# Performance work log

Measured on AMD Instinct MI355X. Metric: run time of the kernel, lower is better.

Reference implementation:

```python
import jax, jax.numpy as jnp
import numpy as np

M, N, K = 4096, 8192, 4096


def setup_inputs() -> dict:
    key = jax.random.key(0)
    k1, k2, k3, k4 = jax.random.split(key, 4)
    a = jax.random.randint(k1, (M, K), 0, 127, dtype=jnp.int32)  # int8 activations
    b = jax.random.randint(k2, (N, K), 0, 127, dtype=jnp.int32)  # int8 weights (row-major [N,K])
    alpha_row = jax.random.uniform(k3, (M, 1), dtype=jnp.float16)  # per-row dequant scale
    alpha_col = jax.random.uniform(k4, (1, N), dtype=jnp.float16)  # per-col dequant scale
    return {"a": a, "b": b, "alpha_row": alpha_row, "alpha_col": alpha_col}


def reference(a, b, alpha_row, alpha_col):
    # x = a @ b.T in fp32 (int8 values upcast), then rescale by outer product of scales
    x = jnp.matmul(a.astype(jnp.float32), b.astype(jnp.float32).T)  # [M, N]
    scale = alpha_row.astype(jnp.float32) * alpha_col.astype(jnp.float32)  # [M, N] via broadcast
    out = x * scale
    return out.astype(jnp.float16)
```

## Files before the change

### kernel.cpp

```cpp
#include <hip/hip_runtime.h>
#include <cstdint>
#include <cstddef>

#define M_DIM 4096
#define N_DIM 8192
#define K_DIM 4096

typedef __attribute__((ext_vector_type(4))) int int4v;
typedef __attribute__((ext_vector_type(16))) int int16v;

__global__ void __launch_bounds__(256) pack_frag(const int* __restrict__ a,
                                                 const int* __restrict__ b,
                                                 unsigned char* __restrict__ pa,
                                                 unsigned char* __restrict__ pb) {
    size_t t = (size_t)blockIdx.x * 256 + threadIdx.x;
    const size_t NA = (size_t)(M_DIM / 32) * (K_DIM / 32) * 64;
    const int* __restrict__ src;
    unsigned char* __restrict__ dst;
    if (t < NA) {
        src = a; dst = pa;
    } else {
        src = b; dst = pb; t -= NA;
    }
    const int l = (int)(t & 63);
    const int s = (int)((t >> 6) & (K_DIM / 32 - 1));
    const int p = (int)(t >> 13);
    const int* g = src + ((size_t)(32 * p + (l & 31))) * K_DIM + s * 32 + (l >> 5) * 16;
    const int4v* g4 = (const int4v*)g;
    int4v o;
#pragma unroll
    for (int q = 0; q < 4; ++q) {
        int4v v = g4[q];
        o[q] = (v[0] & 0xff) | ((v[1] & 0xff) << 8) | ((v[2] & 0xff) << 16) | (v[3] << 24);
    }
    ((int4v*)dst)[t] = o;
}

__device__ inline void async_copy16(const unsigned char* g, unsigned char* l) {
    __builtin_amdgcn_global_load_lds(
        (const __attribute__((address_space(1))) void*)g,
        (__attribute__((address_space(3))) void*)l,
        16, 0, 0);
}

__global__ void __launch_bounds__(512, 2) gemm_i8(const unsigned char* __restrict__ Ap,
                                                  const unsigned char* __restrict__ Bp,
                                                  const _Float16* __restrict__ arow,
                                                  const _Float16* __restrict__ acol,
                                                  _Float16* __restrict__ Cout) {
    __shared__ __align__(16) unsigned char As[4 * 16384];
    __shared__ __align__(16) unsigned char Bs[4 * 16384];

    const int tid  = threadIdx.x;
    const int lane = tid & 63;
    const int wave = tid >> 6;
    const int bn   = blockIdx.x;
    const int bm   = blockIdx.y;

    const int pm0 = (wave & 3) * 2;
    const int pn0 = (wave >> 2) * 4;

    const unsigned char* ag = Ap + (size_t)(bm * 8 + wave) * 131072 + lane * 16;
    const unsigned char* bg = Bp + (size_t)(bn * 8 + wave) * 131072 + lane * 16;
    const int slo = wave * 2048;

    const int a_off = pm0 * 2048 + lane * 16;
    const int b_off = pn0 * 2048 + lane * 16;

    int16v acc[2][4];
#pragma unroll
    for (int i = 0; i < 2; ++i)
#pragma unroll
        for (int j = 0; j < 4; ++j) acc[i][j] = (int16v)0;

    const int NT = K_DIM / 64;

#pragma unroll
    for (int u = 0; u < 2; ++u) {
        async_copy16(ag + u * 1024,        As + slo + u * 1024);
        async_copy16(bg + u * 1024,        Bs + slo + u * 1024);
        async_copy16(ag + 2048 + u * 1024, As + 16384 + slo + u * 1024);
        async_copy16(bg + 2048 + u * 1024, Bs + 16384 + slo + u * 1024);
    }
    __syncthreads();

    for (int T = 0; T < NT; T += 2) {
        if (T + 2 < NT) {
#pragma unroll
            for (int w = 2; w < 4; ++w) {
                const size_t gko = (size_t)(T + w) * 2048;
                const int buf = ((T + w) & 3) * 16384;
#pragma unroll
                for (int u = 0; u < 2; ++u) {
                    async_copy16(ag + gko + u * 1024, As + buf + slo + u * 1024);
                    async_copy16(bg + gko + u * 1024, Bs + buf + slo + u * 1024);
                }
            }
        }

#pragma unroll
        for (int v = 0; v < 2; ++v) {
            const int cur = ((T + v) & 3) * 16384;
            const unsigned char* Ac = As + cur;
            const unsigned char* Bc = Bs + cur;

            int4v af[2][2], bf[2][4];
#pragma unroll
            for (int u = 0; u < 2; ++u) {
#pragma unroll
                for (int i = 0; i < 2; ++i)
                    af[u][i] = *(const int4v*)(Ac + a_off + i * 2048 + u * 1024);
#pragma unroll
                for (int j = 0; j < 4; ++j)
                    bf[u][j] = *(const int4v*)(Bc + b_off + j * 2048 + u * 1024);
            }

#pragma unroll
            for (int u = 0; u < 2; ++u)
#pragma unroll
                for (int i = 0; i < 2; ++i)
#pragma unroll
                    for (int j = 0; j < 4; ++j)
                        acc[i][j] = __builtin_amdgcn_mfma_i32_32x32x32_i8(
                            af[u][i], bf[u][j], acc[i][j], 0, 0, 0);
        }

        __syncthreads();
    }

    const int gcol0 = bn * 256 + pn0 * 32 + (lane & 31);
    float ac4[4];
#pragma unroll
    for (int j = 0; j < 4; ++j) ac4[j] = (float)acol[gcol0 + j * 32];

    const size_t rbase = (size_t)bm * 256 + pm0 * 32 + 4 * (lane >> 5);
#pragma unroll
    for (int i = 0; i < 2; ++i) {
#pragma unroll
        for (int r = 0; r < 16; ++r) {
            const size_t row = rbase + i * 32 + (r & 3) + 8 * (r >> 2);
            const float ar = (float)arow[row];
            _Float16* outp = Cout + row * (size_t)N_DIM + gcol0;
#pragma unroll
            for (int j = 0; j < 4; ++j) {
                float v = (float)acc[i][j][r] * ar * ac4[j];
                outp[j * 32] = (_Float16)v;
            }
        }
    }
}

extern "C" void kernel_launch(void* const* d_in, const int* in_sizes, int n_in,
                              void* d_out, int out_size, void* d_ws, size_t ws_size,
                              hipStream_t stream) {
    const int* a = (const int*)d_in[0];
    const int* b = (const int*)d_in[1];
    const _Float16* ar = (const _Float16*)d_in[2];
    const _Float16* ac = (const _Float16*)d_in[3];
    _Float16* out = (_Float16*)d_out;

    unsigned char* pa = (unsigned char*)d_ws;
    unsigned char* pb = pa + (size_t)M_DIM * K_DIM;

    const size_t total_frag = (size_t)(M_DIM / 32 + N_DIM / 32) * (K_DIM / 32) * 64;
    pack_frag<<<(int)(total_frag / 256), 256, 0, stream>>>(a, b, pa, pb);

    dim3 grid(N_DIM / 256, M_DIM / 256);
    gemm_i8<<<grid, 512, 0, stream>>>(pa, pb, ar, ac, out);
}
```

Measured before the change: 381.7 us.

## Use 4 waves with 128x128 warp tiles and inline-asm MFMA into AGPRs

Halves the block to 256 threads (4 waves), giving each wave a 4x4 grid of 32x32 MFMA tiles instead of 2x4, so each wave does twice the work. Each thread now issues twice as many async copies. All LDS fragments for both k-steps are loaded up front, and MFMAs are issued through inline asm that keeps accumulators in AGPRs. The aim is more MFMA work per LDS read and fewer waves. The cost is much higher register pressure, lower occupancy, and manual hazard nops before the epilogue.

```diff
diff --git a/kernel.cpp b/kernel.cpp
--- a/kernel.cpp
+++ b/kernel.cpp
@@ -43,7 +43,11 @@
         16, 0, 0);
 }
 
-__global__ void __launch_bounds__(512, 2) gemm_i8(const unsigned char* __restrict__ Ap,
+__device__ inline void mfma32(int16v& acc, int4v av, int4v bv) {
+    asm("v_mfma_i32_32x32x32_i8 %0, %1, %2, %0" : "+a"(acc) : "v"(av), "v"(bv));
+}
+
+__global__ void __launch_bounds__(256, 1) gemm_i8(const unsigned char* __restrict__ Ap,
                                                   const unsigned char* __restrict__ Bp,
                                                   const _Float16* __restrict__ arow,
                                                   const _Float16* __restrict__ acol,
@@ -57,31 +61,42 @@
     const int bn   = blockIdx.x;
     const int bm   = blockIdx.y;
 
-    const int pm0 = (wave & 3) * 2;
-    const int pn0 = (wave >> 2) * 4;
+    const int pm0 = (wave & 1) * 4;
+    const int pn0 = (wave >> 1) * 4;
 
-    const unsigned char* ag = Ap + (size_t)(bm * 8 + wave) * 131072 + lane * 16;
-    const unsigned char* bg = Bp + (size_t)(bn * 8 + wave) * 131072 + lane * 16;
-    const int slo = wave * 2048;
+    const unsigned char* ag[2];
+    const unsigned char* bg[2];
+    int slo[2];
+#pragma unroll
+    for (int r = 0; r < 2; ++r) {
+        const int p = 2 * wave + r;
+        ag[r]  = Ap + (size_t)(bm * 8 + p) * 131072 + lane * 16;
+        bg[r]  = Bp + (size_t)(bn * 8 + p) * 131072 + lane * 16;
+        slo[r] = p * 2048;
+    }
 
     const int a_off = pm0 * 2048 + lane * 16;
     const int b_off = pn0 * 2048 + lane * 16;
 
-    int16v acc[2][4];
+    int16v acc[4][4];
 #pragma unroll
-    for (int i = 0; i < 2; ++i)
+    for (int i = 0; i < 4; ++i)
 #pragma unroll
         for (int j = 0; j < 4; ++j) acc[i][j] = (int16v)0;
 
     const int NT = K_DIM / 64;
 
 #pragma unroll
-    for (int u = 0; u < 2; ++u) {
-        async_copy16(ag + u * 1024,        As + slo + u * 1024);
-        async_copy16(bg + u * 1024,        Bs + slo + u * 1024);
-        async_copy16(ag + 2048 + u * 1024, As + 16384 + slo + u * 1024);
-        async_copy16(bg + 2048 + u * 1024, Bs + 16384 + slo + u * 1024);
-    }
+    for (int t = 0; t < 2; ++t)
+#pragma unroll
+        for (int r = 0; r < 2; ++r)
+#pragma unroll
+            for (int u = 0; u < 2; ++u) {
+                async_copy16(ag[r] + t * 2048 + u * 1024,
+                             As + t * 16384 + slo[r] + u * 1024);
+                async_copy16(bg[r] + t * 2048 + u * 1024,
+                             Bs + t * 16384 + slo[r] + u * 1024);
+            }
     __syncthreads();
 
     for (int T = 0; T < NT; T += 2) {
@@ -91,42 +106,53 @@
                 const size_t gko = (size_t)(T + w) * 2048;
                 const int buf = ((T + w) & 3) * 16384;
 #pragma unroll
-                for (int u = 0; u < 2; ++u) {
-                    async_copy16(ag + gko + u * 1024, As + buf + slo + u * 1024);
-                    async_copy16(bg + gko + u * 1024, Bs + buf + slo + u * 1024);
-                }
+                for (int r = 0; r < 2; ++r)
+#pragma unroll
+                    for (int u = 0; u < 2; ++u) {
+                        async_copy16(ag[r] + gko + u * 1024, As + buf + slo[r] + u * 1024);
+                        async_copy16(bg[r] + gko + u * 1024, Bs + buf + slo[r] + u * 1024);
+                    }
             }
         }
 
+        const int c0 = (T & 3) * 16384;
+        const int c1 = ((T + 1) & 3) * 16384;
+
+        int4v a0[8], b0[8], a1[8], b1[8];
 #pragma unroll
-        for (int v = 0; v < 2; ++v) {
-            const int cur = ((T + v) & 3) * 16384;
-            const unsigned char* Ac = As + cur;
-            const unsigned char* Bc = Bs + cur;
-
-            int4v af[2][2], bf[2][4];
+        for (int i = 0; i < 4; ++i)
 #pragma unroll
             for (int u = 0; u < 2; ++u) {
+                a0[i * 2 + u] = *(const int4v*)(As + c0 + a_off + i * 2048 + u * 1024);
+                b0[i * 2 + u] = *(const int4v*)(Bs + c0 + b_off + i * 2048 + u * 1024);
+            }
 #pragma unroll
-                for (int i = 0; i < 2; ++i)
-                    af[u][i] = *(const int4v*)(Ac + a_off + i * 2048 + u * 1024);
+        for (int i = 0; i < 4; ++i)
 #pragma unroll
-                for (int j = 0; j < 4; ++j)
-                    bf[u][j] = *(const int4v*)(Bc + b_off + j * 2048 + u * 1024);
+            for (int u = 0; u < 2; ++u) {
+                a1[i * 2 + u] = *(const int4v*)(As + c1 + a_off + i * 2048 + u * 1024);
+                b1[i * 2 + u] = *(const int4v*)(Bs + c1 + b_off + i * 2048 + u * 1024);
             }
 
 #pragma unroll
-            for (int u = 0; u < 2; ++u)
+        for (int u = 0; u < 2; ++u)
 #pragma unroll
-                for (int i = 0; i < 2; ++i)
+            for (int i = 0; i < 4; ++i)
 #pragma unroll
-                    for (int j = 0; j < 4; ++j)
-                        acc[i][j] = __builtin_amdgcn_mfma_i32_32x32x32_i8(
-                            af[u][i], bf[u][j], acc[i][j], 0, 0, 0);
-        }
+                for (int j = 0; j < 4; ++j)
+                    mfma32(acc[i][j], a0[i * 2 + u], b0[j * 2 + u]);
+#pragma unroll
+        for (int u = 0; u < 2; ++u)
+#pragma unroll
+            for (int i = 0; i < 4; ++i)
+#pragma unroll
+                for (int j = 0; j < 4; ++j)
+                    mfma32(acc[i][j], a1[i * 2 + u], b1[j * 2 + u]);
 
         __syncthreads();
     }
+
+    asm volatile("s_nop 7\n\ts_nop 7" ::);
 
     const int gcol0 = bn * 256 + pn0 * 32 + (lane & 31);
     float ac4[4];
@@ -135,7 +161,7 @@
 
     const size_t rbase = (size_t)bm * 256 + pm0 * 32 + 4 * (lane >> 5);
 #pragma unroll
-    for (int i = 0; i < 2; ++i) {
+    for (int i = 0; i < 4; ++i) {
 #pragma unroll
         for (int r = 0; r < 16; ++r) {
             const size_t row = rbase + i * 32 + (r & 3) + 8 * (r >> 2);
@@ -166,5 +192,5 @@
     pack_frag<<<(int)(total_frag / 256), 256, 0, stream>>>(a, b, pa, pb);
 
     dim3 grid(N_DIM / 256, M_DIM / 256);
-    gemm_i8<<<grid, 512, 0, stream>>>(pa, pb, ar, ac, out);
+    gemm_i8<<<grid, 256, 0, stream>>>(pa, pb, ar, ac, out);
 }
```

Result: slower. 407.0 us (+6.6%).
